# Kernel optimization log

Measured on AMD Instinct MI355X. Metric: run time of the kernel, lower is better.

## Reference

```python
import jax, jax.numpy as jnp
import numpy as np

B, S, D = 4, 2048, 1024
E = 8            # num_experts
F = 4096         # expert hidden dim (4*D)
T = B * S        # tokens
CAP = 1280       # capacity = ceil(1.25 * T / E)


def setup_inputs() -> dict:
    key = jax.random.key(0)
    k1, k2, k3, k4 = jax.random.split(key, 4)
    inputs = jax.random.normal(k1, (B, S, D), dtype=jnp.float32)
    gate_w = jax.random.normal(k2, (D, E), dtype=jnp.float32) / np.sqrt(D)
    w1 = jax.random.normal(k3, (E, D, F), dtype=jnp.float32) / np.sqrt(D)
    w2 = jax.random.normal(k4, (E, F, D), dtype=jnp.float32) / np.sqrt(F)
    return {"inputs": inputs, "gate_w": gate_w, "w1": w1, "w2": w2}


def reference(inputs, gate_w, w1, w2):
    tokens = inputs.reshape(-1, D)                       # [T, D]
    logits = tokens @ gate_w                             # [T, E] (gate, no bias)
    probs = jax.nn.softmax(logits, axis=-1)
    expert_idx = jnp.argmax(probs, axis=-1)              # top-1 routing
    mask1 = jax.nn.one_hot(expert_idx, E, dtype=tokens.dtype)        # [T, E]
    # position of each token within its chosen expert's queue
    pos = (jnp.cumsum(mask1, axis=0) - 1.0).astype(jnp.int32)        # [T, E]
    # one_hot of out-of-range (>= CAP) positions is all-zero -> capacity drop
    sec_mask = mask1[:, :, None] * jax.nn.one_hot(pos, CAP, dtype=tokens.dtype)  # [T, E, C]
    combine_weights = probs[:, :, None] * sec_mask       # [T, E, C]
    # dispatch: matmul(sec_mask.permute(1,2,0), tokens) -> [E, C, D]
    expert_input = jnp.einsum('tec,td->ecd', sec_mask, tokens)
    # grouped per-expert FFN
    h = jax.nn.relu(jnp.einsum('ecd,edf->ecf', expert_input, w1))    # [E, C, F]
    expert_output = jnp.einsum('ecf,efd->ecd', h, w2)                # [E, C, D]
    # combine: [T, E*C] @ [E*C, D]
    out = jnp.einsum('tec,ecd->td', combine_weights, expert_output)  # [T, D]
    return out.reshape(inputs.shape)
```

## Files before the change

kernel.cpp:

```cpp
#include <hip/hip_runtime.h>
#include <hip/hip_bf16.h>

#define TOKENS   8192
#define DDIM     1024
#define NEXP     8
#define FDIM     4096
#define CAPACITY 1280

typedef __attribute__((ext_vector_type(8))) __bf16 bf16x8;
typedef __attribute__((ext_vector_type(4))) __bf16 bf16x4;
typedef __attribute__((ext_vector_type(4))) float  f32x4;

typedef __attribute__((address_space(1))) const void gvoid_t;
typedef __attribute__((address_space(3))) void       lvoid_t;

__device__ __forceinline__ void async16(const void* g, void* l) {
  __builtin_amdgcn_global_load_lds((gvoid_t*)g, (lvoid_t*)l, 16, 0, 0);
}

__global__ void gate_kernel(const float* __restrict__ x, const float* __restrict__ gw,
                            int* __restrict__ eidx, float* __restrict__ prob) {
  const int t = blockIdx.x;
  const int lane = threadIdx.x;
  const float* xp = x + (size_t)t * DDIM;
  float acc[NEXP];
#pragma unroll
  for (int e = 0; e < NEXP; ++e) acc[e] = 0.f;
#pragma unroll 4
  for (int i = 0; i < DDIM / 64; ++i) {
    const int d = i * 64 + lane;
    const float xv = xp[d];
    const f32x4 g0 = *(const f32x4*)(gw + d * NEXP);
    const f32x4 g1 = *(const f32x4*)(gw + d * NEXP + 4);
    acc[0] += xv * g0[0]; acc[1] += xv * g0[1];
    acc[2] += xv * g0[2]; acc[3] += xv * g0[3];
    acc[4] += xv * g1[0]; acc[5] += xv * g1[1];
    acc[6] += xv * g1[2]; acc[7] += xv * g1[3];
  }
#pragma unroll
  for (int e = 0; e < NEXP; ++e) {
    float v = acc[e];
#pragma unroll
    for (int off = 32; off; off >>= 1) v += __shfl_xor(v, off);
    acc[e] = v;
  }
  if (lane == 0) {
    float m = acc[0]; int mi = 0;
#pragma unroll
    for (int e = 1; e < NEXP; ++e) if (acc[e] > m) { m = acc[e]; mi = e; }
    float s = 0.f;
#pragma unroll
    for (int e = 0; e < NEXP; ++e) s += __expf(acc[e] - m);
    eidx[t] = mi;
    prob[t] = 1.f / s;
  }
}

__global__ void scan_kernel(const int* __restrict__ eidx, int* __restrict__ src) {
  __shared__ int buf[2][NEXP][256];
  const int tid = threadIdx.x;
  for (int i = tid; i < NEXP * CAPACITY; i += 256) src[i] = -1;
  const int t0 = tid * (TOKENS / 256);
#pragma unroll
  for (int e = 0; e < NEXP; ++e) buf[0][e][tid] = 0;
  for (int k = 0; k < TOKENS / 256; ++k) {
    const int e = eidx[t0 + k];
    buf[0][e][tid]++;
  }
  __syncthreads();
  int cur = 0;
  for (int off = 1; off < 256; off <<= 1) {
#pragma unroll
    for (int e = 0; e < NEXP; ++e) {
      int v = buf[cur][e][tid];
      if (tid >= off) v += buf[cur][e][tid - off];
      buf[cur ^ 1][e][tid] = v;
    }
    __syncthreads();
    cur ^= 1;
  }
#pragma unroll
  for (int e = 0; e < NEXP; ++e)
    buf[cur ^ 1][e][tid] = (tid > 0) ? buf[cur][e][tid - 1] : 0;
  for (int k = 0; k < TOKENS / 256; ++k) {
    const int t = t0 + k;
    const int e = eidx[t];
    const int p = buf[cur ^ 1][e][tid]++;
    if (p < CAPACITY) src[e * CAPACITY + p] = t;
  }
}

__global__ void dispatch_kernel(const float* __restrict__ tokens, const int* __restrict__ src,
                                __bf16* __restrict__ Xb) {
  const int slot = blockIdx.x;
  const int tid  = threadIdx.x;
  const int t = src[slot];
  bf16x4* dst = (bf16x4*)(Xb + (size_t)slot * DDIM);
  bf16x4 o;
  if (t >= 0) {
    const f32x4 v = ((const f32x4*)(tokens + (size_t)t * DDIM))[tid];
    o[0] = (__bf16)v[0]; o[1] = (__bf16)v[1]; o[2] = (__bf16)v[2]; o[3] = (__bf16)v[3];
  } else {
    o[0] = (__bf16)0.f; o[1] = (__bf16)0.f; o[2] = (__bf16)0.f; o[3] = (__bf16)0.f;
  }
  dst[tid] = o;
}

__global__ void transpose_convert_kernel(const float* __restrict__ w, __bf16* __restrict__ wt,
                                         int R, int C) {
  __shared__ __bf16 tile[64][65];
  const int e = blockIdx.z;
  const float* wp = w + (size_t)e * R * C;
  __bf16* op = wt + (size_t)e * R * C;
  const int c0 = blockIdx.x * 64, r0 = blockIdx.y * 64;
  const int tx = threadIdx.x, ty = threadIdx.y;
#pragma unroll
  for (int i = 0; i < 16; ++i) {
    const int r = ty + i * 4;
    tile[r][tx] = (__bf16)wp[(size_t)(r0 + r) * C + c0 + tx];
  }
  __syncthreads();
#pragma unroll
  for (int i = 0; i < 16; ++i) {
    const int cc = ty + i * 4;
    op[(size_t)(c0 + cc) * R + r0 + tx] = tile[tx][cc];
  }
}

template <int MODE>
__global__ __launch_bounds__(256, 2)
void gemm_kernel(const __bf16* __restrict__ A, const __bf16* __restrict__ B,
                 __bf16* __restrict__ Cbf, float* __restrict__ out,
                 const int* __restrict__ src, const float* __restrict__ prob,
                 int N, int K, size_t sA, size_t sB, size_t sC) {
  __shared__ __bf16 lds[2][128 * 64];
  const int e  = blockIdx.z;
  const int n0 = blockIdx.x * 128;
  const int m0 = blockIdx.y * 128;
  const __bf16* Ae = A + (size_t)e * sA;
  const __bf16* Be = B + (size_t)e * sB;
  const int tid = threadIdx.x;
  const int wave = tid >> 6, lane = tid & 63;
  const int wr = wave >> 1, wc = wave & 1;
  const int rl = lane & 15, gl = lane >> 4;
  const f32x4 zero = {0.f, 0.f, 0.f, 0.f};
  f32x4 acc[4][4];
#pragma unroll
  for (int m = 0; m < 4; ++m)
#pragma unroll
    for (int n = 0; n < 4; ++n) acc[m][n] = zero;

  for (int kt = 0; kt < K; kt += 64) {
#pragma unroll
    for (int i = 0; i < 4; ++i) {
      const int s   = (wave * 4 + i) * 64 + lane;
      const int row = s >> 3;
      const int cg  = (s & 7) ^ (row & 7);
      async16(Ae + (size_t)(m0 + row) * K + kt + cg * 8, &lds[0][(wave * 4 + i) * 512]);
      async16(Be + (size_t)(n0 + row) * K + kt + cg * 8, &lds[1][(wave * 4 + i) * 512]);
    }
    __syncthreads();
    const char* la = (const char*)&lds[0][0];
    const char* lb = (const char*)&lds[1][0];
#pragma unroll
    for (int kk = 0; kk < 2; ++kk) {
      bf16x8 af[4], bfv[4];
#pragma unroll
      for (int m = 0; m < 4; ++m) {
        const int row = wr * 64 + m * 16 + rl;
        const int g = (kk * 4 + gl) ^ (row & 7);
        af[m] = *(const bf16x8*)(la + row * 128 + g * 16);
      }
#pragma unroll
      for (int n = 0; n < 4; ++n) {
        const int row = wc * 64 + n * 16 + rl;
        const int g = (kk * 4 + gl) ^ (row & 7);
        bfv[n] = *(const bf16x8*)(lb + row * 128 + g * 16);
      }
#pragma unroll
      for (int m = 0; m < 4; ++m)
#pragma unroll
        for (int n = 0; n < 4; ++n)
          acc[m][n] = __builtin_amdgcn_mfma_f32_16x16x32_bf16(af[m], bfv[n], acc[m][n], 0, 0, 0);
    }
    __syncthreads();
  }

  if (MODE == 0) {
    __bf16* Ce = Cbf + (size_t)e * sC;
#pragma unroll
    for (int m = 0; m < 4; ++m)
#pragma unroll
      for (int j = 0; j < 4; ++j) {
        const int row = m0 + wr * 64 + m * 16 + gl * 4 + j;
#pragma unroll
        for (int n = 0; n < 4; ++n) {
          const int col = n0 + wc * 64 + n * 16 + rl;
          float v = acc[m][n][j];
          v = v > 0.f ? v : 0.f;
          Ce[(size_t)row * N + col] = (__bf16)v;
        }
      }
  } else {
#pragma unroll
    for (int m = 0; m < 4; ++m)
#pragma unroll
      for (int j = 0; j < 4; ++j) {
        const int slot = m0 + wr * 64 + m * 16 + gl * 4 + j;
        const int t = src[e * CAPACITY + slot];
        if (t >= 0) {
          const float p = prob[t];
          float* op = out + (size_t)t * N;
#pragma unroll
          for (int n = 0; n < 4; ++n) {
            const int col = n0 + wc * 64 + n * 16 + rl;
            op[col] = p * acc[m][n][j];
          }
        }
      }
  }
}

extern "C" void kernel_launch(void* const* d_in, const int* in_sizes, int n_in,
                              void* d_out, int out_size, void* d_ws, size_t ws_size,
                              hipStream_t stream) {
  const float* x  = (const float*)d_in[0];
  const float* gw = (const float*)d_in[1];
  const float* w1 = (const float*)d_in[2];
  const float* w2 = (const float*)d_in[3];
  float* out = (float*)d_out;

  char* ws = (char*)d_ws;
  size_t off = 0;
  auto alloc = [&](size_t bytes) {
    void* p = ws + off;
    off += (bytes + 255) & ~(size_t)255;
    return p;
  };
  __bf16* W1bT = (__bf16*)alloc((size_t)NEXP * FDIM * DDIM * 2);
  __bf16* W2bT = (__bf16*)alloc((size_t)NEXP * DDIM * FDIM * 2);
  __bf16* Xb   = (__bf16*)alloc((size_t)NEXP * CAPACITY * DDIM * 2);
  __bf16* Hb   = (__bf16*)alloc((size_t)NEXP * CAPACITY * FDIM * 2);
  int*   eidx  = (int*)alloc(TOKENS * sizeof(int));
  float* prob  = (float*)alloc(TOKENS * sizeof(float));
  int*   srcm  = (int*)alloc(NEXP * CAPACITY * sizeof(int));
  (void)ws_size; (void)in_sizes; (void)n_in;

  hipMemsetAsync(d_out, 0, (size_t)out_size * sizeof(float), stream);

  gate_kernel<<<TOKENS, 64, 0, stream>>>(x, gw, eidx, prob);
  scan_kernel<<<1, 256, 0, stream>>>(eidx, srcm);
  dispatch_kernel<<<NEXP * CAPACITY, 256, 0, stream>>>(x, srcm, Xb);
  transpose_convert_kernel<<<dim3(FDIM / 64, DDIM / 64, NEXP), dim3(64, 4), 0, stream>>>(
      w1, W1bT, DDIM, FDIM);
  transpose_convert_kernel<<<dim3(DDIM / 64, FDIM / 64, NEXP), dim3(64, 4), 0, stream>>>(
      w2, W2bT, FDIM, DDIM);
  gemm_kernel<0><<<dim3(FDIM / 128, CAPACITY / 128, NEXP), 256, 0, stream>>>(
      Xb, W1bT, Hb, nullptr, nullptr, nullptr,
      FDIM, DDIM, (size_t)CAPACITY * DDIM, (size_t)FDIM * DDIM, (size_t)CAPACITY * FDIM);
  gemm_kernel<1><<<dim3(DDIM / 128, CAPACITY / 128, NEXP), 256, 0, stream>>>(
      Hb, W2bT, nullptr, out, srcm, prob,
      DDIM, FDIM, (size_t)CAPACITY * FDIM, (size_t)DDIM * FDIM, 0);
}
```

Baseline: 335.5 us.

## Use 256-row 8-wave GEMM tiles with double-buffered LDS and skip empty capacity tiles

Replaces the 128x128 four-wave expert GEMM with an eight-wave kernel that computes 256-row tiles (256x256 for the first FFN GEMM, 256x128 for the second). Global-to-LDS loads are double-buffered with explicit vmcnt waits so the next K-tile loads while the current one is multiplied, and MFMA sections run at raised wave priority. The scan kernel now writes per-expert token counts, so GEMM workgroups whose row tile lies wholly beyond an expert's occupied slots exit early. Workgroup IDs are also remapped to spread experts across the grid. The trade-off is larger LDS and register use per workgroup, which may cut occupancy, and manual waitcnt logic that must stay exactly matched to the number of issued loads.

```diff
diff --git a/kernel.cpp b/kernel.cpp
--- a/kernel.cpp
+++ b/kernel.cpp
@@ -6,6 +6,7 @@
 #define NEXP     8
 #define FDIM     4096
 #define CAPACITY 1280
+#define NYT      5
 
 typedef __attribute__((ext_vector_type(8))) __bf16 bf16x8;
 typedef __attribute__((ext_vector_type(4))) __bf16 bf16x4;
@@ -56,7 +57,8 @@
   }
 }
 
-__global__ void scan_kernel(const int* __restrict__ eidx, int* __restrict__ src) {
+__global__ void scan_kernel(const int* __restrict__ eidx, int* __restrict__ src,
+                            int* __restrict__ counts) {
   __shared__ int buf[2][NEXP][256];
   const int tid = threadIdx.x;
   for (int i = tid; i < NEXP * CAPACITY; i += 256) src[i] = -1;
@@ -79,6 +81,7 @@
     __syncthreads();
     cur ^= 1;
   }
+  if (tid < NEXP) counts[tid] = buf[cur][tid][255];
 #pragma unroll
   for (int e = 0; e < NEXP; ++e)
     buf[cur ^ 1][e][tid] = (tid > 0) ? buf[cur][e][tid - 1] : 0;
@@ -127,75 +130,135 @@
   }
 }
 
-template <int MODE>
-__global__ __launch_bounds__(256, 2)
-void gemm_kernel(const __bf16* __restrict__ A, const __bf16* __restrict__ B,
-                 __bf16* __restrict__ Cbf, float* __restrict__ out,
-                 const int* __restrict__ src, const float* __restrict__ prob,
-                 int N, int K, size_t sA, size_t sB, size_t sC) {
-  __shared__ __bf16 lds[2][128 * 64];
-  const int e  = blockIdx.z;
-  const int n0 = blockIdx.x * 128;
-  const int m0 = blockIdx.y * 128;
+template <int BN, int MODE>
+__global__ __launch_bounds__(512, 2)
+void gemm8_kernel(const __bf16* __restrict__ A, const __bf16* __restrict__ B,
+                  __bf16* __restrict__ Cbf, float* __restrict__ out,
+                  const int* __restrict__ src, const float* __restrict__ prob,
+                  const int* __restrict__ counts,
+                  int K, size_t sA, size_t sB, size_t sC) {
+  constexpr int N   = (MODE == 0) ? FDIM : DDIM;
+  constexpr int NX  = N / BN;
+  constexpr int HB  = BN / 128;
+  constexpr int NF  = BN / 64;
+  constexpr int WNC = 16 * NF;
+  __shared__ char lds[64 * 1024 + BN * 256];
+  char* ldsA = lds;
+  char* ldsB = lds + 64 * 1024;
+
+  const int nwg = NX * NYT * NEXP;
+  int wg = blockIdx.x;
+  wg = (wg & 7) * (nwg >> 3) + (wg >> 3);
+  const int e   = wg / (NX * NYT);
+  const int rem = wg - e * (NX * NYT);
+  const int ty  = rem % NYT;
+  const int tx  = rem / NYT;
+  const int m0  = ty * 256, n0 = tx * BN;
+
+  const int cnt   = counts[e];
+  const int tiles = (cnt + 255) >> 8;
+  if (ty >= ((tiles < NYT) ? tiles : NYT)) return;
+
   const __bf16* Ae = A + (size_t)e * sA;
   const __bf16* Be = B + (size_t)e * sB;
   const int tid = threadIdx.x;
-  const int wave = tid >> 6, lane = tid & 63;
-  const int wr = wave >> 1, wc = wave & 1;
+  const int wid = tid >> 6, lane = tid & 63;
+  const int wm = wid >> 2, wn = wid & 3;
   const int rl = lane & 15, gl = lane >> 4;
-  const f32x4 zero = {0.f, 0.f, 0.f, 0.f};
-  f32x4 acc[4][4];
-#pragma unroll
-  for (int m = 0; m < 4; ++m)
-#pragma unroll
-    for (int n = 0; n < 4; ++n) acc[m][n] = zero;
-
-  for (int kt = 0; kt < K; kt += 64) {
-#pragma unroll
-    for (int i = 0; i < 4; ++i) {
-      const int s   = (wave * 4 + i) * 64 + lane;
-      const int row = s >> 3;
-      const int cg  = (s & 7) ^ (row & 7);
-      async16(Ae + (size_t)(m0 + row) * K + kt + cg * 8, &lds[0][(wave * 4 + i) * 512]);
-      async16(Be + (size_t)(n0 + row) * K + kt + cg * 8, &lds[1][(wave * 4 + i) * 512]);
+
+  f32x4 acc[8][NF];
+#pragma unroll
+  for (int m = 0; m < 8; ++m)
+#pragma unroll
+    for (int n = 0; n < NF; ++n) acc[m][n] = (f32x4){0.f, 0.f, 0.f, 0.f};
+
+  auto stage = [&](int c, int kt) {
+    const int k0 = kt * 64;
+#pragma unroll
+    for (int h = 0; h < 2; ++h)
+#pragma unroll
+      for (int i = 0; i < 2; ++i) {
+        const int s = i * 512 + tid, row = s >> 3, cg = (s & 7) ^ (row & 7);
+        async16(Ae + (size_t)(m0 + h * 128 + row) * K + k0 + cg * 8,
+                ldsA + (c * 2 + h) * 16384 + s * 16);
+      }
+#pragma unroll
+    for (int h = 0; h < HB; ++h)
+#pragma unroll
+      for (int i = 0; i < 2; ++i) {
+        const int s = i * 512 + tid, row = s >> 3, cg = (s & 7) ^ (row & 7);
+        async16(Be + (size_t)(n0 + h * 128 + row) * K + k0 + cg * 8,
+                ldsB + (c * HB + h) * 16384 + s * 16);
+      }
+  };
+
+  auto phase = [&](int c, int kk) {
+    bf16x8 af[8], bv[NF];
+#pragma unroll
+    for (int m = 0; m < 8; ++m) {
+      const int rowin = m * 16 + rl;
+      af[m] = *(const bf16x8*)(ldsA + (c * 2 + wm) * 16384 + rowin * 128 +
+                               (((kk * 4 + gl) ^ (rowin & 7)) * 16));
     }
-    __syncthreads();
-    const char* la = (const char*)&lds[0][0];
-    const char* lb = (const char*)&lds[1][0];
-#pragma unroll
-    for (int kk = 0; kk < 2; ++kk) {
-      bf16x8 af[4], bfv[4];
-#pragma unroll
-      for (int m = 0; m < 4; ++m) {
-        const int row = wr * 64 + m * 16 + rl;
-        const int g = (kk * 4 + gl) ^ (row & 7);
-        af[m] = *(const bf16x8*)(la + row * 128 + g * 16);
-      }
-#pragma unroll
-      for (int n = 0; n < 4; ++n) {
-        const int row = wc * 64 + n * 16 + rl;
-        const int g = (kk * 4 + gl) ^ (row & 7);
-        bfv[n] = *(const bf16x8*)(lb + row * 128 + g * 16);
-      }
-#pragma unroll
-      for (int m = 0; m < 4; ++m)
-#pragma unroll
-        for (int n = 0; n < 4; ++n)
-          acc[m][n] = __builtin_amdgcn_mfma_f32_16x16x32_bf16(af[m], bfv[n], acc[m][n], 0, 0, 0);
+#pragma unroll
+    for (int n = 0; n < NF; ++n) {
+      const int rowB = wn * WNC + n * 16 + rl;
+      const int h = rowB >> 7, rowin = rowB & 127;
+      bv[n] = *(const bf16x8*)(ldsB + (c * HB + h) * 16384 + rowin * 128 +
+                               (((kk * 4 + gl) ^ (rowin & 7)) * 16));
     }
-    __syncthreads();
-  }
+    __builtin_amdgcn_s_setprio(1);
+#pragma unroll
+    for (int m = 0; m < 8; ++m)
+#pragma unroll
+      for (int n = 0; n < NF; ++n)
+        acc[m][n] = __builtin_amdgcn_mfma_f32_16x16x32_bf16(af[m], bv[n], acc[m][n], 0, 0, 0);
+    __builtin_amdgcn_s_setprio(0);
+  };
+
+#define WAIT_TOT() do { if constexpr (HB == 2) \
+      asm volatile("s_waitcnt vmcnt(8)" ::: "memory"); \
+    else asm volatile("s_waitcnt vmcnt(6)" ::: "memory"); } while (0)
+
+  const int nkt = K >> 6;
+  stage(0, 0);
+  stage(1, 1);
+  WAIT_TOT();
+  asm volatile("" ::: "memory");
+  __builtin_amdgcn_s_barrier();
+  asm volatile("" ::: "memory");
+
+  for (int t = 0; t < nkt; ++t) {
+    const int c = t & 1;
+    phase(c, 0);
+    phase(c, 1);
+    if (t + 1 < nkt) {
+      asm volatile("" ::: "memory");
+      __builtin_amdgcn_s_barrier();
+      asm volatile("" ::: "memory");
+      if (t + 2 < nkt) {
+        stage(c, t + 2);
+        WAIT_TOT();
+      } else {
+        asm volatile("s_waitcnt vmcnt(0)" ::: "memory");
+      }
+      asm volatile("" ::: "memory");
+      __builtin_amdgcn_s_barrier();
+      asm volatile("" ::: "memory");
+    }
+  }
+#undef WAIT_TOT
 
   if (MODE == 0) {
     __bf16* Ce = Cbf + (size_t)e * sC;
 #pragma unroll
-    for (int m = 0; m < 4; ++m)
+    for (int m = 0; m < 8; ++m)
 #pragma unroll
       for (int j = 0; j < 4; ++j) {
-        const int row = m0 + wr * 64 + m * 16 + gl * 4 + j;
-#pragma unroll
-        for (int n = 0; n < 4; ++n) {
-          const int col = n0 + wc * 64 + n * 16 + rl;
+        const int row = m0 + wm * 128 + m * 16 + gl * 4 + j;
+#pragma unroll
+        for (int n = 0; n < NF; ++n) {
+          const int col = n0 + wn * WNC + n * 16 + rl;
           float v = acc[m][n][j];
           v = v > 0.f ? v : 0.f;
           Ce[(size_t)row * N + col] = (__bf16)v;
@@ -203,17 +266,17 @@
       }
   } else {
 #pragma unroll
-    for (int m = 0; m < 4; ++m)
+    for (int m = 0; m < 8; ++m)
 #pragma unroll
       for (int j = 0; j < 4; ++j) {
-        const int slot = m0 + wr * 64 + m * 16 + gl * 4 + j;
+        const int slot = m0 + wm * 128 + m * 16 + gl * 4 + j;
         const int t = src[e * CAPACITY + slot];
         if (t >= 0) {
           const float p = prob[t];
           float* op = out + (size_t)t * N;
 #pragma unroll
-          for (int n = 0; n < 4; ++n) {
-            const int col = n0 + wc * 64 + n * 16 + rl;
+          for (int n = 0; n < NF; ++n) {
+            const int col = n0 + wn * WNC + n * 16 + rl;
             op[col] = p * acc[m][n][j];
           }
         }
@@ -244,21 +307,22 @@
   int*   eidx  = (int*)alloc(TOKENS * sizeof(int));
   float* prob  = (float*)alloc(TOKENS * sizeof(float));
   int*   srcm  = (int*)alloc(NEXP * CAPACITY * sizeof(int));
+  int*   cnts  = (int*)alloc(NEXP * sizeof(int));
   (void)ws_size; (void)in_sizes; (void)n_in;
 
   hipMemsetAsync(d_out, 0, (size_t)out_size * sizeof(float), stream);
 
   gate_kernel<<<TOKENS, 64, 0, stream>>>(x, gw, eidx, prob);
-  scan_kernel<<<1, 256, 0, stream>>>(eidx, srcm);
+  scan_kernel<<<1, 256, 0, stream>>>(eidx, srcm, cnts);
   dispatch_kernel<<<NEXP * CAPACITY, 256, 0, stream>>>(x, srcm, Xb);
   transpose_convert_kernel<<<dim3(FDIM / 64, DDIM / 64, NEXP), dim3(64, 4), 0, stream>>>(
       w1, W1bT, DDIM, FDIM);
   transpose_convert_kernel<<<dim3(DDIM / 64, FDIM / 64, NEXP), dim3(64, 4), 0, stream>>>(
       w2, W2bT, FDIM, DDIM);
-  gemm_kernel<0><<<dim3(FDIM / 128, CAPACITY / 128, NEXP), 256, 0, stream>>>(
-      Xb, W1bT, Hb, nullptr, nullptr, nullptr,
-      FDIM, DDIM, (size_t)CAPACITY * DDIM, (size_t)FDIM * DDIM, (size_t)CAPACITY * FDIM);
-  gemm_kernel<1><<<dim3(DDIM / 128, CAPACITY / 128, NEXP), 256, 0, stream>>>(
-      Hb, W2bT, nullptr, out, srcm, prob,
-      DDIM, FDIM, (size_t)CAPACITY * FDIM, (size_t)DDIM * FDIM, 0);
-}
+  gemm8_kernel<256, 0><<<(FDIM / 256) * NYT * NEXP, 512, 0, stream>>>(
+      Xb, W1bT, Hb, nullptr, nullptr, nullptr, cnts,
+      DDIM, (size_t)CAPACITY * DDIM, (size_t)FDIM * DDIM, (size_t)CAPACITY * FDIM);
+  gemm8_kernel<128, 1><<<(DDIM / 128) * NYT * NEXP, 512, 0, stream>>>(
+      Hb, W2bT, nullptr, out, srcm, prob, cnts,
+      FDIM, (size_t)CAPACITY * FDIM, (size_t)DDIM * FDIM, 0);
+}
```

New measurement: 385.7 us. 15.0% more time.

## Double-buffer GEMM LDS, skip empty expert tiles, and remap workgroups across XCDs

Applied to the files above, without the earlier changes.

The grouped GEMM now double-buffers its LDS tiles, issuing the async global-to-LDS loads for the next K step while MFMAs run on the current one. It drops from two barriers per K step to one and raises wave priority around the MFMA block. The scan kernel exports per-expert token counts, and GEMM workgroups whose row tile lies beyond an expert's filled slots exit early, skipping padded capacity rows. A 1D grid with an XCD-aware workgroup remap replaces the 3D grid. LDS use doubles to 64KB per block, which may limit occupancy under launch_bounds(256,2).

```diff
diff --git a/kernel.cpp b/kernel.cpp
--- a/kernel.cpp
+++ b/kernel.cpp
@@ -6,6 +6,7 @@
 #define NEXP     8
 #define FDIM     4096
 #define CAPACITY 1280
+#define NYT      10
 
 typedef __attribute__((ext_vector_type(8))) __bf16 bf16x8;
 typedef __attribute__((ext_vector_type(4))) __bf16 bf16x4;
@@ -56,7 +57,8 @@
   }
 }
 
-__global__ void scan_kernel(const int* __restrict__ eidx, int* __restrict__ src) {
+__global__ void scan_kernel(const int* __restrict__ eidx, int* __restrict__ src,
+                            int* __restrict__ counts) {
   __shared__ int buf[2][NEXP][256];
   const int tid = threadIdx.x;
   for (int i = tid; i < NEXP * CAPACITY; i += 256) src[i] = -1;
@@ -79,6 +81,7 @@
     __syncthreads();
     cur ^= 1;
   }
+  if (tid < NEXP) counts[tid] = buf[cur][tid][255];
 #pragma unroll
   for (int e = 0; e < NEXP; ++e)
     buf[cur ^ 1][e][tid] = (tid > 0) ? buf[cur][e][tid - 1] : 0;
@@ -132,58 +135,82 @@
 void gemm_kernel(const __bf16* __restrict__ A, const __bf16* __restrict__ B,
                  __bf16* __restrict__ Cbf, float* __restrict__ out,
                  const int* __restrict__ src, const float* __restrict__ prob,
-                 int N, int K, size_t sA, size_t sB, size_t sC) {
-  __shared__ __bf16 lds[2][128 * 64];
-  const int e  = blockIdx.z;
-  const int n0 = blockIdx.x * 128;
-  const int m0 = blockIdx.y * 128;
+                 const int* __restrict__ counts,
+                 int K, size_t sA, size_t sB, size_t sC) {
+  constexpr int N  = (MODE == 0) ? FDIM : DDIM;
+  constexpr int NX = N / 128;
+  __shared__ char lds[2][32768];
+
+  const int nwg = NX * NYT * NEXP;
+  int wg = blockIdx.x;
+  wg = (wg & 7) * (nwg >> 3) + (wg >> 3);
+  const int e   = wg / (NX * NYT);
+  const int rem = wg - e * (NX * NYT);
+  const int ty  = rem % NYT;
+  const int tx  = rem / NYT;
+  const int m0  = ty * 128, n0 = tx * 128;
+
+  const int cnt   = counts[e];
+  const int tiles = (cnt + 127) >> 7;
+  if (ty >= ((tiles < NYT) ? tiles : NYT)) return;
+
   const __bf16* Ae = A + (size_t)e * sA;
   const __bf16* Be = B + (size_t)e * sB;
   const int tid = threadIdx.x;
-  const int wave = tid >> 6, lane = tid & 63;
-  const int wr = wave >> 1, wc = wave & 1;
+  const int wid = tid >> 6, lane = tid & 63;
+  const int wm = wid >> 1, wn = wid & 1;
   const int rl = lane & 15, gl = lane >> 4;
-  const f32x4 zero = {0.f, 0.f, 0.f, 0.f};
+  const int wu = __builtin_amdgcn_readfirstlane(tid) >> 6;
+
   f32x4 acc[4][4];
 #pragma unroll
   for (int m = 0; m < 4; ++m)
 #pragma unroll
-    for (int n = 0; n < 4; ++n) acc[m][n] = zero;
-
-  for (int kt = 0; kt < K; kt += 64) {
+    for (int n = 0; n < 4; ++n) acc[m][n] = (f32x4){0.f, 0.f, 0.f, 0.f};
+
+  auto stage = [&](int c, int kt) {
+    const int k0 = kt * 64;
 #pragma unroll
     for (int i = 0; i < 4; ++i) {
-      const int s   = (wave * 4 + i) * 64 + lane;
-      const int row = s >> 3;
-      const int cg  = (s & 7) ^ (row & 7);
-      async16(Ae + (size_t)(m0 + row) * K + kt + cg * 8, &lds[0][(wave * 4 + i) * 512]);
-      async16(Be + (size_t)(n0 + row) * K + kt + cg * 8, &lds[1][(wave * 4 + i) * 512]);
-    }
-    __syncthreads();
-    const char* la = (const char*)&lds[0][0];
-    const char* lb = (const char*)&lds[1][0];
-#pragma unroll
-    for (int kk = 0; kk < 2; ++kk) {
-      bf16x8 af[4], bfv[4];
-#pragma unroll
-      for (int m = 0; m < 4; ++m) {
-        const int row = wr * 64 + m * 16 + rl;
-        const int g = (kk * 4 + gl) ^ (row & 7);
-        af[m] = *(const bf16x8*)(la + row * 128 + g * 16);
-      }
-#pragma unroll
-      for (int n = 0; n < 4; ++n) {
-        const int row = wc * 64 + n * 16 + rl;
-        const int g = (kk * 4 + gl) ^ (row & 7);
-        bfv[n] = *(const bf16x8*)(lb + row * 128 + g * 16);
-      }
-#pragma unroll
-      for (int m = 0; m < 4; ++m)
-#pragma unroll
-        for (int n = 0; n < 4; ++n)
-          acc[m][n] = __builtin_amdgcn_mfma_f32_16x16x32_bf16(af[m], bfv[n], acc[m][n], 0, 0, 0);
-    }
-    __syncthreads();
+      const int chunk = i * 4 + wu;
+      const int s = chunk * 64 + lane;
+      const int row = s >> 3, cg = (s & 7) ^ (row & 7);
+      async16(Ae + (size_t)(m0 + row) * K + k0 + cg * 8, &lds[c][chunk * 1024]);
+      async16(Be + (size_t)(n0 + row) * K + k0 + cg * 8, &lds[c][16384 + chunk * 1024]);
+    }
+  };
+
+  auto phase = [&](int c, int kk) {
+    bf16x8 af[4], bv[4];
+#pragma unroll
+    for (int m = 0; m < 4; ++m) {
+      const int rowin = wm * 64 + m * 16 + rl;
+      af[m] = *(const bf16x8*)(&lds[c][rowin * 128 + (((kk * 4 + gl) ^ (rowin & 7)) * 16)]);
+    }
+#pragma unroll
+    for (int n = 0; n < 4; ++n) {
+      const int rowin = wn * 64 + n * 16 + rl;
+      bv[n] = *(const bf16x8*)(&lds[c][16384 + rowin * 128 +
+                                       (((kk * 4 + gl) ^ (rowin & 7)) * 16)]);
+    }
+    __builtin_amdgcn_s_setprio(1);
+#pragma unroll
+    for (int m = 0; m < 4; ++m)
+#pragma unroll
+      for (int n = 0; n < 4; ++n)
+        acc[m][n] = __builtin_amdgcn_mfma_f32_16x16x32_bf16(af[m], bv[n], acc[m][n], 0, 0, 0);
+    __builtin_amdgcn_s_setprio(0);
+  };
+
+  const int nkt = K >> 6;
+  stage(0, 0);
+  __syncthreads();
+  for (int t = 0; t < nkt; ++t) {
+    const int cur = t & 1;
+    if (t + 1 < nkt) stage(cur ^ 1, t + 1);
+    phase(cur, 0);
+    phase(cur, 1);
+    if (t + 1 < nkt) __syncthreads();
   }
 
   if (MODE == 0) {
@@ -192,10 +219,10 @@
     for (int m = 0; m < 4; ++m)
 #pragma unroll
       for (int j = 0; j < 4; ++j) {
-        const int row = m0 + wr * 64 + m * 16 + gl * 4 + j;
+        const int row = m0 + wm * 64 + m * 16 + gl * 4 + j;
 #pragma unroll
         for (int n = 0; n < 4; ++n) {
-          const int col = n0 + wc * 64 + n * 16 + rl;
+          const int col = n0 + wn * 64 + n * 16 + rl;
           float v = acc[m][n][j];
           v = v > 0.f ? v : 0.f;
           Ce[(size_t)row * N + col] = (__bf16)v;
@@ -206,14 +233,14 @@
     for (int m = 0; m < 4; ++m)
 #pragma unroll
       for (int j = 0; j < 4; ++j) {
-        const int slot = m0 + wr * 64 + m * 16 + gl * 4 + j;
+        const int slot = m0 + wm * 64 + m * 16 + gl * 4 + j;
         const int t = src[e * CAPACITY + slot];
         if (t >= 0) {
           const float p = prob[t];
           float* op = out + (size_t)t * N;
 #pragma unroll
           for (int n = 0; n < 4; ++n) {
-            const int col = n0 + wc * 64 + n * 16 + rl;
+            const int col = n0 + wn * 64 + n * 16 + rl;
             op[col] = p * acc[m][n][j];
           }
         }
@@ -244,21 +271,22 @@
   int*   eidx  = (int*)alloc(TOKENS * sizeof(int));
   float* prob  = (float*)alloc(TOKENS * sizeof(float));
   int*   srcm  = (int*)alloc(NEXP * CAPACITY * sizeof(int));
+  int*   cnts  = (int*)alloc(NEXP * sizeof(int));
   (void)ws_size; (void)in_sizes; (void)n_in;
 
   hipMemsetAsync(d_out, 0, (size_t)out_size * sizeof(float), stream);
 
   gate_kernel<<<TOKENS, 64, 0, stream>>>(x, gw, eidx, prob);
-  scan_kernel<<<1, 256, 0, stream>>>(eidx, srcm);
+  scan_kernel<<<1, 256, 0, stream>>>(eidx, srcm, cnts);
   dispatch_kernel<<<NEXP * CAPACITY, 256, 0, stream>>>(x, srcm, Xb);
   transpose_convert_kernel<<<dim3(FDIM / 64, DDIM / 64, NEXP), dim3(64, 4), 0, stream>>>(
       w1, W1bT, DDIM, FDIM);
   transpose_convert_kernel<<<dim3(DDIM / 64, FDIM / 64, NEXP), dim3(64, 4), 0, stream>>>(
       w2, W2bT, FDIM, DDIM);
-  gemm_kernel<0><<<dim3(FDIM / 128, CAPACITY / 128, NEXP), 256, 0, stream>>>(
-      Xb, W1bT, Hb, nullptr, nullptr, nullptr,
-      FDIM, DDIM, (size_t)CAPACITY * DDIM, (size_t)FDIM * DDIM, (size_t)CAPACITY * FDIM);
-  gemm_kernel<1><<<dim3(DDIM / 128, CAPACITY / 128, NEXP), 256, 0, stream>>>(
-      Hb, W2bT, nullptr, out, srcm, prob,
-      DDIM, FDIM, (size_t)CAPACITY * FDIM, (size_t)DDIM * FDIM, 0);
-}
+  gemm_kernel<0><<<(FDIM / 128) * NYT * NEXP, 256, 0, stream>>>(
+      Xb, W1bT, Hb, nullptr, nullptr, nullptr, cnts,
+      DDIM, (size_t)CAPACITY * DDIM, (size_t)FDIM * DDIM, (size_t)CAPACITY * FDIM);
+  gemm_kernel<1><<<(DDIM / 128) * NYT * NEXP, 256, 0, stream>>>(
+      Hb, W2bT, nullptr, out, srcm, prob, cnts,
+      FDIM, (size_t)CAPACITY * FDIM, (size_t)DDIM * FDIM, 0);
+}
```

Measured after the change: 366.9 us. 9.3% more time.
